# Kernel tuning notes

Measured on AMD Instinct MI355X. Metric: run time of the kernel, lower is better.

## Reference

```python
import jax, jax.numpy as jnp
import numpy as np

B, L, D_MODEL = 16, 2048, 512
S, D_LLM = 1000, 1024
H, E = 8, 64  # n_heads, d_keys
D_OUT = 64


def setup_inputs() -> dict:
    key = jax.random.key(0)
    ks = jax.random.split(key, 11)
    sc = lambda d: 1.0 / np.sqrt(d)
    return {
        "target_embedding": jax.random.normal(ks[0], (B, L, D_MODEL), dtype=jnp.float32),
        "source_embedding": jax.random.normal(ks[1], (S, D_LLM), dtype=jnp.float32),
        "value_embedding": jax.random.normal(ks[2], (S, D_LLM), dtype=jnp.float32),
        "Wq": jax.random.normal(ks[3], (D_MODEL, H * E), dtype=jnp.float32) * sc(D_MODEL),
        "bq": jnp.zeros((H * E,), dtype=jnp.float32),
        "Wk": jax.random.normal(ks[4], (D_LLM, H * E), dtype=jnp.float32) * sc(D_LLM),
        "bk": jnp.zeros((H * E,), dtype=jnp.float32),
        "Wv": jax.random.normal(ks[5], (D_LLM, H * E), dtype=jnp.float32) * sc(D_LLM),
        "bv": jnp.zeros((H * E,), dtype=jnp.float32),
        "Wo": jax.random.normal(ks[6], (H * E, D_OUT), dtype=jnp.float32) * sc(H * E),
        "bo": jnp.zeros((D_OUT,), dtype=jnp.float32),
    }


def reference(target_embedding, source_embedding, value_embedding,
              Wq, bq, Wk, bk, Wv, bv, Wo, bo):
    # projections
    q = (target_embedding @ Wq + bq).reshape(B, L, H, E)   # blhe
    k = (source_embedding @ Wk + bk).reshape(S, H, E)      # she
    v = (value_embedding @ Wv + bv).reshape(S, H, E)       # she
    scale = 1.0 / jnp.sqrt(jnp.asarray(E, dtype=q.dtype))
    scores = jnp.einsum("blhe,she->bhls", q, k)            # (B,H,L,S)
    A = jax.nn.softmax(scale * scores, axis=-1)            # dropout in eval mode = identity
    out = jnp.einsum("bhls,she->blhe", A, v).reshape(B, L, H * E)
    return out @ Wo + bo                                    # (B,L,64)
```

## Files before the change

kernel.cpp:

```cpp
#include <hip/hip_runtime.h>

typedef __attribute__((ext_vector_type(4))) float  f32x4;
typedef __attribute__((ext_vector_type(8))) __bf16 bf16x8;
typedef __attribute__((ext_vector_type(4))) __bf16 bf16x4;

static __device__ __forceinline__ f32x4 mfma16(bf16x8 a, bf16x8 b, f32x4 c) {
  return __builtin_amdgcn_mfma_f32_16x16x32_bf16(a, b, c, 0, 0, 0);
}

typedef __attribute__((address_space(1))) const unsigned int* gas1_t;
typedef __attribute__((address_space(3))) unsigned int* las3_t;
static __device__ __forceinline__ void glds16(const void* g, void* l) {
  __builtin_amdgcn_global_load_lds((gas1_t)g, (las3_t)l, 16, 0, 0);
}

#define QSCALE 0.18033688011112042f

__global__ __launch_bounds__(256) void prep_wT(
    const float* __restrict__ Wq, const float* __restrict__ Wk,
    const float* __restrict__ Wv, const float* __restrict__ Wo,
    __bf16* __restrict__ wqT, __bf16* __restrict__ wkT,
    __bf16* __restrict__ wvT, __bf16* __restrict__ woT) {
  __shared__ float tile[32][33];
  const int t = blockIdx.x;
  const float* in; __bf16* out; int K, N, tk, tn;
  if (t < 256)       { in = Wq; out = wqT; K = 512;  N = 512; tk = t & 15;          tn = t >> 4; }
  else if (t < 768)  { in = Wk; out = wkT; K = 1024; N = 512; tk = (t-256) & 31;    tn = (t-256) >> 5; }
  else if (t < 1280) { in = Wv; out = wvT; K = 1024; N = 512; tk = (t-768) & 31;    tn = (t-768) >> 5; }
  else               { in = Wo; out = woT; K = 512;  N = 64;  tk = (t-1280) & 15;   tn = (t-1280) >> 4; }
  const int k0 = tk * 32, n0 = tn * 32;
  const int c = threadIdx.x & 31, r = threadIdx.x >> 5;
#pragma unroll
  for (int i = 0; i < 4; ++i)
    tile[r + i * 8][c] = in[(size_t)(k0 + r + i * 8) * N + n0 + c];
  __syncthreads();
#pragma unroll
  for (int i = 0; i < 4; ++i)
    out[(size_t)(n0 + r + i * 8) * K + k0 + c] = (__bf16)tile[c][r + i * 8];
}

__global__ __launch_bounds__(256) void prep_cvt(
    const float* __restrict__ tgt, const float* __restrict__ src,
    const float* __restrict__ val,
    __bf16* __restrict__ tgtb, __bf16* __restrict__ srcb, __bf16* __restrict__ valb) {
  const int j = blockIdx.x * 256 + threadIdx.x;
  const int C0 = 32768 * 512 / 4;
  const int CV = 1024 * 1024 / 4;
  if (j < C0) {
    f32x4 v = *(const f32x4*)&tgt[(size_t)j * 4];
    bf16x4 o; o[0]=(__bf16)v[0]; o[1]=(__bf16)v[1]; o[2]=(__bf16)v[2]; o[3]=(__bf16)v[3];
    *(bf16x4*)&tgtb[(size_t)j * 4] = o;
  } else if (j < C0 + 2 * CV) {
    const int which = (j - C0) / CV;
    const int u = (j - C0) - which * CV;
    const float* in = which ? val : src;
    __bf16* outp = which ? valb : srcb;
    bf16x4 o;
    if (u * 4 < 1000 * 1024) {
      f32x4 v = *(const f32x4*)&in[(size_t)u * 4];
      o[0]=(__bf16)v[0]; o[1]=(__bf16)v[1]; o[2]=(__bf16)v[2]; o[3]=(__bf16)v[3];
    } else {
      o[0]=(__bf16)0.0f; o[1]=(__bf16)0.0f; o[2]=(__bf16)0.0f; o[3]=(__bf16)0.0f;
    }
    *(bf16x4*)&outp[(size_t)u * 4] = o;
  }
}

template <int MODE>
__global__ __launch_bounds__(256, 2) void gemm_bt(
    const __bf16* __restrict__ A, const __bf16* __restrict__ BT,
    const float* __restrict__ bias, float scale,
    __bf16* __restrict__ C, int M, int N, int K) {
  const int n0 = blockIdx.x * 128, m0 = blockIdx.y * 128;
  __shared__ __bf16 sA[2][128 * 32], sB[2][128 * 32];
  const int t = threadIdx.x;
  const int w = t >> 6, lane = t & 63;
  const int wr = w >> 1, wc = w & 1;
  const int lr = lane & 15, lg = lane >> 4;

  const int grow = w * 32 + (lane >> 2);
  const int lslot = (lane & 3) ^ ((lane >> 2) & 3) ^ (lane >> 4);
  const int woff = w * 2048;

  const int rslot = (lg ^ (lr & 3) ^ ((lr >> 2) & 3)) << 4;
  const int aOff = wr * 4096 + lr * 64 + rslot;
  const int bOff = wc * 4096 + lr * 64 + rslot;

  f32x4 acc[4][4];
#pragma unroll
  for (int i = 0; i < 4; ++i)
#pragma unroll
    for (int j = 0; j < 4; ++j) acc[i][j] = f32x4{0.f, 0.f, 0.f, 0.f};

  const size_t gaBase0 = (size_t)(m0 + grow) * K + lslot * 8;
  const size_t gaBase1 = (size_t)(m0 + grow + 16) * K + lslot * 8;
  const size_t gbBase0 = (size_t)(n0 + grow) * K + lslot * 8;
  const size_t gbBase1 = (size_t)(n0 + grow + 16) * K + lslot * 8;

  glds16(&A[gaBase0], (char*)sA[0] + woff);
  glds16(&A[gaBase1], (char*)sA[0] + woff + 1024);
  glds16(&BT[gbBase0], (char*)sB[0] + woff);
  glds16(&BT[gbBase1], (char*)sB[0] + woff + 1024);
  __syncthreads();

  const int NK = K >> 5;
  for (int it = 0; it < NK; ++it) {
    const int cur = it & 1;
    if (it + 1 < NK) {
      const int kc = (it + 1) << 5;
      glds16(&A[gaBase0 + kc], (char*)sA[cur ^ 1] + woff);
      glds16(&A[gaBase1 + kc], (char*)sA[cur ^ 1] + woff + 1024);
      glds16(&BT[gbBase0 + kc], (char*)sB[cur ^ 1] + woff);
      glds16(&BT[gbBase1 + kc], (char*)sB[cur ^ 1] + woff + 1024);
    }
    bf16x8 af[4], bfr[4];
#pragma unroll
    for (int i = 0; i < 4; ++i) {
      af[i]  = *(const bf16x8*)((const char*)sA[cur] + aOff + i * 1024);
      bfr[i] = *(const bf16x8*)((const char*)sB[cur] + bOff + i * 1024);
    }
    __builtin_amdgcn_s_setprio(1);
#pragma unroll
    for (int i = 0; i < 4; ++i)
#pragma unroll
      for (int j = 0; j < 4; ++j) acc[i][j] = mfma16(af[i], bfr[j], acc[i][j]);
    __builtin_amdgcn_s_setprio(0);
    __syncthreads();
  }

#pragma unroll
  for (int i = 0; i < 4; ++i) {
    const int rowb = m0 + wr * 64 + i * 16 + lg * 4;
#pragma unroll
    for (int j = 0; j < 4; ++j) {
      const int col = n0 + wc * 64 + j * 16 + lr;
      const float bb = bias ? bias[col] : 0.0f;
      if (MODE == 0) {
#pragma unroll
        for (int r = 0; r < 4; ++r)
          C[(size_t)(rowb + r) * N + col] = (__bf16)((acc[i][j][r] + bb) * scale);
      } else {
        bf16x4 v;
#pragma unroll
        for (int r = 0; r < 4; ++r) v[r] = (__bf16)((acc[i][j][r] + bb) * scale);
        *(bf16x4*)&C[(size_t)col * M + rowb] = v;
      }
    }
  }
}

__global__ __launch_bounds__(256, 3) void attn_kernel(
    const __bf16* __restrict__ qg, const __bf16* __restrict__ kg,
    const __bf16* __restrict__ vtg, __bf16* __restrict__ og) {
  const int bid = blockIdx.x;
  const int lt = bid & 15, h = (bid >> 4) & 7, b = bid >> 7;
  const int w = threadIdx.x >> 6, lane = threadIdx.x & 63;
  const int lr = lane & 15, g = lane >> 4, lr7 = lane & 7;
  const int l0 = lt * 128 + w * 32;

  __shared__ __bf16 sK[2][4096];
  __shared__ __bf16 sV[2][4096];
  __shared__ __bf16 sP[4][1024];
  char* const pbase = (char*)&sP[w][0];

  const int srowi = lane >> 3;
  const int sslot = (lane & 7) ^ srowi;
  const int krow = w * 16 + srowi;
  const size_t kgBase = (size_t)krow * 512 + h * 64 + sslot * 8;
  const size_t vgBase = (size_t)(h * 64 + krow) * 1024 + sslot * 8;

  bf16x8 qf[2][2];
#pragma unroll
  for (int qi = 0; qi < 2; ++qi)
#pragma unroll
    for (int hf = 0; hf < 2; ++hf)
      qf[qi][hf] = *(const bf16x8*)&qg[
          ((size_t)b * 2048 + l0 + qi * 16 + lr) * 512 + h * 64 + hf * 32 + g * 8];

  f32x4 o[2][4], lsacc[2];
#pragma unroll
  for (int qi = 0; qi < 2; ++qi) {
#pragma unroll
    for (int j = 0; j < 4; ++j) o[qi][j] = f32x4{0.f, 0.f, 0.f, 0.f};
    lsacc[qi] = f32x4{0.f, 0.f, 0.f, 0.f};
  }

  bf16x8 ones8;
#pragma unroll
  for (int i = 0; i < 8; ++i) ones8[i] = (__bf16)1.0f;

  const int eOff0 = lr * 128 + ((g ^ lr7) << 4);
  const int pswz = lr7 << 4;

  glds16(&kg[kgBase], (char*)&sK[0][0] + w * 2048);
  glds16(&kg[kgBase + (size_t)8 * 512], (char*)&sK[0][0] + w * 2048 + 1024);
  glds16(&vtg[vgBase], (char*)&sV[0][0] + w * 2048);
  glds16(&vtg[vgBase + (size_t)8 * 1024], (char*)&sV[0][0] + w * 2048 + 1024);
  __syncthreads();

  for (int sc = 0; sc < 16; ++sc) {
    const int p = sc & 1;
    if (sc < 15) {
      const int sn = (sc + 1) * 64;
      char* nk = (char*)&sK[p ^ 1][0] + w * 2048;
      char* nv = (char*)&sV[p ^ 1][0] + w * 2048;
      glds16(&kg[kgBase + (size_t)sn * 512], nk);
      glds16(&kg[kgBase + (size_t)(sn + 8) * 512], nk + 1024);
      glds16(&vtg[vgBase + sn], nv);
      glds16(&vtg[vgBase + sn + 8 * 1024], nv + 1024);
    }
    const char* kbuf = (const char*)&sK[p][0];
    const char* vbuf = (const char*)&sV[p][0];

    f32x4 d[2][4];
#pragma unroll
    for (int t = 0; t < 4; ++t) {
      const bf16x8 kf0 = *(const bf16x8*)(kbuf + t * 2048 + eOff0);
      const bf16x8 kf1 = *(const bf16x8*)(kbuf + t * 2048 + (eOff0 ^ 64));
      __builtin_amdgcn_s_setprio(1);
#pragma unroll
      for (int qi = 0; qi < 2; ++qi) {
        f32x4 z = {0.f, 0.f, 0.f, 0.f};
        z = mfma16(kf0, qf[qi][0], z);
        z = mfma16(kf1, qf[qi][1], z);
        d[qi][t] = z;
      }
      __builtin_amdgcn_s_setprio(0);
    }
    if (sc == 15) {
#pragma unroll
      for (int qi = 0; qi < 2; ++qi)
#pragma unroll
        for (int t = 0; t < 4; ++t)
#pragma unroll
          for (int r = 0; r < 4; ++r)
            if (960 + t * 16 + 4 * g + r >= 1000) d[qi][t][r] = -1.0e30f;
    }

#pragma unroll
    for (int qi = 0; qi < 2; ++qi) {
#pragma unroll
      for (int t = 0; t < 4; ++t) {
        bf16x4 pv;
        pv[0] = (__bf16)exp2f(d[qi][t][0]);
        pv[1] = (__bf16)exp2f(d[qi][t][1]);
        pv[2] = (__bf16)exp2f(d[qi][t][2]);
        pv[3] = (__bf16)exp2f(d[qi][t][3]);
        *(bf16x4*)(pbase + lr * 128 + ((t * 32 + g * 8) ^ pswz)) = pv;
      }
#pragma unroll
      for (int kc = 0; kc < 2; ++kc) {
        bf16x8 vf0 = *(const bf16x8*)(vbuf + 0 * 2048 + (eOff0 ^ (kc * 64)));
        bf16x8 vf1 = *(const bf16x8*)(vbuf + 1 * 2048 + (eOff0 ^ (kc * 64)));
        bf16x8 vf2 = *(const bf16x8*)(vbuf + 2 * 2048 + (eOff0 ^ (kc * 64)));
        bf16x8 vf3 = *(const bf16x8*)(vbuf + 3 * 2048 + (eOff0 ^ (kc * 64)));
        const bf16x8 pB = *(const bf16x8*)(
            pbase + lr * 128 + ((kc * 64 + g * 16) ^ pswz));
        __builtin_amdgcn_s_setprio(1);
        lsacc[qi] = mfma16(ones8, pB, lsacc[qi]);
        o[qi][0] = mfma16(vf0, pB, o[qi][0]);
        o[qi][1] = mfma16(vf1, pB, o[qi][1]);
        o[qi][2] = mfma16(vf2, pB, o[qi][2]);
        o[qi][3] = mfma16(vf3, pB, o[qi][3]);
        __builtin_amdgcn_s_setprio(0);
      }
    }
    __syncthreads();
  }

  const int rr = lane >> 2, cc = lane & 3;
  const int rsw = (rr & 7) << 4;
#pragma unroll
  for (int qi = 0; qi < 2; ++qi) {
    const float rinv = 1.0f / lsacc[qi][0];
#pragma unroll
    for (int j = 0; j < 4; ++j) {
      bf16x4 v;
#pragma unroll
      for (int r = 0; r < 4; ++r) v[r] = (__bf16)(o[qi][j][r] * rinv);
      *(bf16x4*)(pbase + lr * 128 + ((j * 32 + g * 8) ^ pswz)) = v;
    }
    const uint4 lo = *(const uint4*)(pbase + rr * 128 + ((cc * 16) ^ rsw));
    const uint4 hi = *(const uint4*)(pbase + rr * 128 + ((cc * 16 + 64) ^ rsw));
    char* orow = (char*)&og[((size_t)b * 2048 + l0 + qi * 16 + rr) * 512 + h * 64];
    *(uint4*)(orow + cc * 16) = lo;
    *(uint4*)(orow + cc * 16 + 64) = hi;
  }
}

__global__ __launch_bounds__(256) void out_proj(
    const __bf16* __restrict__ ab, const __bf16* __restrict__ woT,
    const float* __restrict__ bo, float* __restrict__ out) {
  const int w = threadIdx.x >> 6, lane = threadIdx.x & 63;
  const int lr = lane & 15, g = lane >> 4;
  const int r0 = blockIdx.x * 64 + w * 16;
  f32x4 acc[4];
#pragma unroll
  for (int j = 0; j < 4; ++j) acc[j] = f32x4{0.f, 0.f, 0.f, 0.f};
  for (int kc = 0; kc < 512; kc += 32) {
    const bf16x8 af = *(const bf16x8*)&ab[(size_t)(r0 + lr) * 512 + kc + g * 8];
#pragma unroll
    for (int j = 0; j < 4; ++j) {
      const bf16x8 bf = *(const bf16x8*)&woT[(size_t)(j * 16 + lr) * 512 + kc + g * 8];
      acc[j] = mfma16(af, bf, acc[j]);
    }
  }
#pragma unroll
  for (int j = 0; j < 4; ++j) {
    const int col = j * 16 + lr;
    const float bb = bo[col];
#pragma unroll
    for (int r = 0; r < 4; ++r)
      out[(size_t)(r0 + 4 * g + r) * 64 + col] = acc[j][r] + bb;
  }
}

extern "C" void kernel_launch(void* const* d_in, const int* in_sizes, int n_in,
                              void* d_out, int out_size, void* d_ws, size_t ws_size,
                              hipStream_t stream) {
  const float* tgt = (const float*)d_in[0];
  const float* src = (const float*)d_in[1];
  const float* val = (const float*)d_in[2];
  const float* Wq  = (const float*)d_in[3];
  const float* bq  = (const float*)d_in[4];
  const float* Wk  = (const float*)d_in[5];
  const float* bk  = (const float*)d_in[6];
  const float* Wv  = (const float*)d_in[7];
  const float* bv  = (const float*)d_in[8];
  const float* Wo  = (const float*)d_in[9];
  const float* bo  = (const float*)d_in[10];
  float* out = (float*)d_out;
  char* ws = (char*)d_ws;

  __bf16* wqT  = (__bf16*)(ws + 0);
  __bf16* wkT  = (__bf16*)(ws + 524288);
  __bf16* wvT  = (__bf16*)(ws + 1572864);
  __bf16* woT  = (__bf16*)(ws + 2621440);
  __bf16* srcb = (__bf16*)(ws + 2686976);
  __bf16* valb = (__bf16*)(ws + 4784128);
  __bf16* kb   = (__bf16*)(ws + 6881280);
  __bf16* vtb  = (__bf16*)(ws + 7929856);
  __bf16* tgtb = (__bf16*)(ws + 8978432);
  __bf16* attnb= (__bf16*)(ws + 8978432);
  __bf16* qb   = (__bf16*)(ws + 42532864);

  prep_wT<<<1312, 256, 0, stream>>>(Wq, Wk, Wv, Wo, wqT, wkT, wvT, woT);
  prep_cvt<<<18432, 256, 0, stream>>>(tgt, src, val, tgtb, srcb, valb);

  gemm_bt<0><<<dim3(4, 256), 256, 0, stream>>>(tgtb, wqT, bq, QSCALE, qb, 32768, 512, 512);
  gemm_bt<0><<<dim3(4, 8), 256, 0, stream>>>(srcb, wkT, bk, 1.0f, kb, 1024, 512, 1024);
  gemm_bt<1><<<dim3(4, 8), 256, 0, stream>>>(valb, wvT, bv, 1.0f, vtb, 1024, 512, 1024);

  attn_kernel<<<2048, 256, 0, stream>>>(qb, kb, vtb, attnb);

  out_proj<<<512, 256, 0, stream>>>(attnb, woT, bo, out);
}
```

Baseline: 315.7 us.

## Fuse fp32-to-bf16 input conversion into GEMM loads and widen attention blocks to 8 waves

The separate prep_cvt pass is removed. The projection GEMMs now read fp32 activations directly, convert them to bf16 in registers and write them into LDS, zero-padding rows past 1000 for K and V. This avoids writing and re-reading a 32 MB bf16 copy of the target embedding, at the cost of the A operand no longer using async global-to-LDS loads. Separately, attention blocks grow to 512 threads (8 waves, 256 query rows), so each staged K/V tile is shared by twice as many waves and each wave issues half as many loads.

```diff
diff --git a/kernel.cpp b/kernel.cpp
--- a/kernel.cpp
+++ b/kernel.cpp
@@ -39,36 +39,9 @@
     out[(size_t)(n0 + r + i * 8) * K + k0 + c] = (__bf16)tile[c][r + i * 8];
 }
 
-__global__ __launch_bounds__(256) void prep_cvt(
-    const float* __restrict__ tgt, const float* __restrict__ src,
-    const float* __restrict__ val,
-    __bf16* __restrict__ tgtb, __bf16* __restrict__ srcb, __bf16* __restrict__ valb) {
-  const int j = blockIdx.x * 256 + threadIdx.x;
-  const int C0 = 32768 * 512 / 4;
-  const int CV = 1024 * 1024 / 4;
-  if (j < C0) {
-    f32x4 v = *(const f32x4*)&tgt[(size_t)j * 4];
-    bf16x4 o; o[0]=(__bf16)v[0]; o[1]=(__bf16)v[1]; o[2]=(__bf16)v[2]; o[3]=(__bf16)v[3];
-    *(bf16x4*)&tgtb[(size_t)j * 4] = o;
-  } else if (j < C0 + 2 * CV) {
-    const int which = (j - C0) / CV;
-    const int u = (j - C0) - which * CV;
-    const float* in = which ? val : src;
-    __bf16* outp = which ? valb : srcb;
-    bf16x4 o;
-    if (u * 4 < 1000 * 1024) {
-      f32x4 v = *(const f32x4*)&in[(size_t)u * 4];
-      o[0]=(__bf16)v[0]; o[1]=(__bf16)v[1]; o[2]=(__bf16)v[2]; o[3]=(__bf16)v[3];
-    } else {
-      o[0]=(__bf16)0.0f; o[1]=(__bf16)0.0f; o[2]=(__bf16)0.0f; o[3]=(__bf16)0.0f;
-    }
-    *(bf16x4*)&outp[(size_t)u * 4] = o;
-  }
-}
-
-template <int MODE>
-__global__ __launch_bounds__(256, 2) void gemm_bt(
-    const __bf16* __restrict__ A, const __bf16* __restrict__ BT,
+template <int MODE, int PADM>
+__global__ __launch_bounds__(256, 2) void gemm_f32a(
+    const float* __restrict__ A32, const __bf16* __restrict__ BT,
     const float* __restrict__ bias, float scale,
     __bf16* __restrict__ C, int M, int N, int K) {
   const int n0 = blockIdx.x * 128, m0 = blockIdx.y * 128;
@@ -78,9 +51,20 @@
   const int wr = w >> 1, wc = w & 1;
   const int lr = lane & 15, lg = lane >> 4;
 
-  const int grow = w * 32 + (lane >> 2);
+  const int growB = w * 32 + (lane >> 2);
   const int lslot = (lane & 3) ^ ((lane >> 2) & 3) ^ (lane >> 4);
   const int woff = w * 2048;
+  const size_t gbBase0 = (size_t)(n0 + growB) * K + lslot * 8;
+  const size_t gbBase1 = (size_t)(n0 + growB + 16) * K + lslot * 8;
+
+  const int arow = w * 32 + (lane >> 1);
+  const int as0 = 2 * (lane & 1);
+  const int aps0 = as0 ^ ((lane >> 1) & 3) ^ ((lane >> 3) & 3);
+  const int aps1 = aps0 ^ 1;
+  const int aWr0 = arow * 64 + aps0 * 16;
+  const int aWr1 = arow * 64 + aps1 * 16;
+  const size_t aBase = (size_t)(m0 + arow) * K + as0 * 8;
+  const bool arowOK = !PADM || (m0 + arow < 1000);
 
   const int rslot = (lg ^ (lr & 3) ^ ((lr >> 2) & 3)) << 4;
   const int aOff = wr * 4096 + lr * 64 + rslot;
@@ -92,13 +76,27 @@
 #pragma unroll
     for (int j = 0; j < 4; ++j) acc[i][j] = f32x4{0.f, 0.f, 0.f, 0.f};
 
-  const size_t gaBase0 = (size_t)(m0 + grow) * K + lslot * 8;
-  const size_t gaBase1 = (size_t)(m0 + grow + 16) * K + lslot * 8;
-  const size_t gbBase0 = (size_t)(n0 + grow) * K + lslot * 8;
-  const size_t gbBase1 = (size_t)(n0 + grow + 16) * K + lslot * 8;
-
-  glds16(&A[gaBase0], (char*)sA[0] + woff);
-  glds16(&A[gaBase1], (char*)sA[0] + woff + 1024);
+  auto stageA = [&](int kc, int buf) {
+    bf16x8 o0, o1;
+    if (arowOK) {
+      const f32x4 a00 = *(const f32x4*)&A32[aBase + kc + 0];
+      const f32x4 a01 = *(const f32x4*)&A32[aBase + kc + 4];
+      const f32x4 a10 = *(const f32x4*)&A32[aBase + kc + 8];
+      const f32x4 a11 = *(const f32x4*)&A32[aBase + kc + 12];
+#pragma unroll
+      for (int e = 0; e < 4; ++e) {
+        o0[e] = (__bf16)a00[e]; o0[4 + e] = (__bf16)a01[e];
+        o1[e] = (__bf16)a10[e]; o1[4 + e] = (__bf16)a11[e];
+      }
+    } else {
+#pragma unroll
+      for (int e = 0; e < 8; ++e) { o0[e] = (__bf16)0.0f; o1[e] = (__bf16)0.0f; }
+    }
+    *(bf16x8*)((char*)sA[buf] + aWr0) = o0;
+    *(bf16x8*)((char*)sA[buf] + aWr1) = o1;
+  };
+
+  stageA(0, 0);
   glds16(&BT[gbBase0], (char*)sB[0] + woff);
   glds16(&BT[gbBase1], (char*)sB[0] + woff + 1024);
   __syncthreads();
@@ -108,10 +106,9 @@
     const int cur = it & 1;
     if (it + 1 < NK) {
       const int kc = (it + 1) << 5;
-      glds16(&A[gaBase0 + kc], (char*)sA[cur ^ 1] + woff);
-      glds16(&A[gaBase1 + kc], (char*)sA[cur ^ 1] + woff + 1024);
       glds16(&BT[gbBase0 + kc], (char*)sB[cur ^ 1] + woff);
       glds16(&BT[gbBase1 + kc], (char*)sB[cur ^ 1] + woff + 1024);
+      stageA(kc, cur ^ 1);
     }
     bf16x8 af[4], bfr[4];
 #pragma unroll
@@ -149,23 +146,23 @@
   }
 }
 
-__global__ __launch_bounds__(256, 3) void attn_kernel(
+__global__ __launch_bounds__(512, 6) void attn_kernel(
     const __bf16* __restrict__ qg, const __bf16* __restrict__ kg,
     const __bf16* __restrict__ vtg, __bf16* __restrict__ og) {
   const int bid = blockIdx.x;
-  const int lt = bid & 15, h = (bid >> 4) & 7, b = bid >> 7;
+  const int lt = bid & 7, h = (bid >> 3) & 7, b = bid >> 6;
   const int w = threadIdx.x >> 6, lane = threadIdx.x & 63;
   const int lr = lane & 15, g = lane >> 4, lr7 = lane & 7;
-  const int l0 = lt * 128 + w * 32;
+  const int l0 = lt * 256 + w * 32;
 
   __shared__ __bf16 sK[2][4096];
   __shared__ __bf16 sV[2][4096];
-  __shared__ __bf16 sP[4][1024];
+  __shared__ __bf16 sP[8][1024];
   char* const pbase = (char*)&sP[w][0];
 
   const int srowi = lane >> 3;
-  const int sslot = (lane & 7) ^ srowi;
-  const int krow = w * 16 + srowi;
+  const int sslot = lr7 ^ srowi;
+  const int krow = w * 8 + srowi;
   const size_t kgBase = (size_t)krow * 512 + h * 64 + sslot * 8;
   const size_t vgBase = (size_t)(h * 64 + krow) * 1024 + sslot * 8;
 
@@ -192,22 +189,16 @@
   const int eOff0 = lr * 128 + ((g ^ lr7) << 4);
   const int pswz = lr7 << 4;
 
-  glds16(&kg[kgBase], (char*)&sK[0][0] + w * 2048);
-  glds16(&kg[kgBase + (size_t)8 * 512], (char*)&sK[0][0] + w * 2048 + 1024);
-  glds16(&vtg[vgBase], (char*)&sV[0][0] + w * 2048);
-  glds16(&vtg[vgBase + (size_t)8 * 1024], (char*)&sV[0][0] + w * 2048 + 1024);
+  glds16(&kg[kgBase], (char*)&sK[0][0] + w * 1024);
+  glds16(&vtg[vgBase], (char*)&sV[0][0] + w * 1024);
   __syncthreads();
 
   for (int sc = 0; sc < 16; ++sc) {
     const int p = sc & 1;
     if (sc < 15) {
       const int sn = (sc + 1) * 64;
-      char* nk = (char*)&sK[p ^ 1][0] + w * 2048;
-      char* nv = (char*)&sV[p ^ 1][0] + w * 2048;
-      glds16(&kg[kgBase + (size_t)sn * 512], nk);
-      glds16(&kg[kgBase + (size_t)(sn + 8) * 512], nk + 1024);
-      glds16(&vtg[vgBase + sn], nv);
-      glds16(&vtg[vgBase + sn + 8 * 1024], nv + 1024);
+      glds16(&kg[kgBase + (size_t)sn * 512], (char*)&sK[p ^ 1][0] + w * 1024);
+      glds16(&vtg[vgBase + sn], (char*)&sV[p ^ 1][0] + w * 1024);
     }
     const char* kbuf = (const char*)&sK[p][0];
     const char* vbuf = (const char*)&sV[p][0];
@@ -336,22 +327,18 @@
   __bf16* wkT  = (__bf16*)(ws + 524288);
   __bf16* wvT  = (__bf16*)(ws + 1572864);
   __bf16* woT  = (__bf16*)(ws + 2621440);
-  __bf16* srcb = (__bf16*)(ws + 2686976);
-  __bf16* valb = (__bf16*)(ws + 4784128);
-  __bf16* kb   = (__bf16*)(ws + 6881280);
-  __bf16* vtb  = (__bf16*)(ws + 7929856);
-  __bf16* tgtb = (__bf16*)(ws + 8978432);
-  __bf16* attnb= (__bf16*)(ws + 8978432);
-  __bf16* qb   = (__bf16*)(ws + 42532864);
+  __bf16* kb   = (__bf16*)(ws + 2686976);
+  __bf16* vtb  = (__bf16*)(ws + 3735552);
+  __bf16* attnb= (__bf16*)(ws + 4784128);
+  __bf16* qb   = (__bf16*)(ws + 38338560);
 
   prep_wT<<<1312, 256, 0, stream>>>(Wq, Wk, Wv, Wo, wqT, wkT, wvT, woT);
-  prep_cvt<<<18432, 256, 0, stream>>>(tgt, src, val, tgtb, srcb, valb);
-
-  gemm_bt<0><<<dim3(4, 256), 256, 0, stream>>>(tgtb, wqT, bq, QSCALE, qb, 32768, 512, 512);
-  gemm_bt<0><<<dim3(4, 8), 256, 0, stream>>>(srcb, wkT, bk, 1.0f, kb, 1024, 512, 1024);
-  gemm_bt<1><<<dim3(4, 8), 256, 0, stream>>>(valb, wvT, bv, 1.0f, vtb, 1024, 512, 1024);
-
-  attn_kernel<<<2048, 256, 0, stream>>>(qb, kb, vtb, attnb);
+
+  gemm_f32a<0, 0><<<dim3(4, 256), 256, 0, stream>>>(tgt, wqT, bq, QSCALE, qb, 32768, 512, 512);
+  gemm_f32a<0, 1><<<dim3(4, 8), 256, 0, stream>>>(src, wkT, bk, 1.0f, kb, 1024, 512, 1024);
+  gemm_f32a<1, 1><<<dim3(4, 8), 256, 0, stream>>>(val, wvT, bv, 1.0f, vtb, 1024, 512, 1024);
+
+  attn_kernel<<<1024, 512, 0, stream>>>(qb, kb, vtb, attnb);
 
   out_proj<<<512, 256, 0, stream>>>(attnb, woT, bo, out);
 }
```

Result: slower. 702.9 us (+122.6%).
